# Optimization experiments

Measured on AMD Instinct MI355X. Metric: run time of the kernel, lower is better.

The kernel has to match this reference:

```python
import jax, jax.numpy as jnp
import numpy as np

EPS = 1e-5
PROJ_EPS = 1e-5
MAX_TANH_ARG = 15.0
NUM_LAYERS = 2

def _norm(x):
    return jnp.sqrt(jnp.sum(x * x, axis=-1, keepdims=True))

def log_map_zero(y):
    # Poincare ball log map at the origin: arctanh(||y||) * y / ||y||
    n = _norm(y)
    n_c = jnp.clip(n, EPS, 1.0 - PROJ_EPS)
    return jnp.arctanh(n_c) * y / jnp.maximum(n, EPS)

def exp_map_zero(v):
    # Poincare ball exp map at the origin: tanh(||v||) * v / ||v||
    n = _norm(v)
    n_c = jnp.clip(n, EPS, MAX_TANH_ARG)
    return jnp.tanh(n_c) * v / jnp.maximum(n, EPS)

def setup_inputs() -> dict:
    key = jax.random.key(0)
    k1, k2, k3, k4 = jax.random.split(key, 4)
    N, K, D = 50000, 32, 128
    # scale initial features so they lie inside the unit ball
    node_repr = jax.random.normal(k1, (N, D), dtype=jnp.float32) * 0.01
    adj_mat = jax.random.randint(k2, (N, K), 0, N, dtype=jnp.int32)
    weight = jax.random.uniform(k3, (N, K), dtype=jnp.float32)
    mask = jnp.ones((N, 1), dtype=jnp.float32)
    # learned params: one [D, D] matrix per layer (tie_weight=False, poincare)
    msg_weights = jax.random.normal(k4, (NUM_LAYERS, D, D), dtype=jnp.float32) * (1.0 / np.sqrt(D))
    return {"node_repr": node_repr, "adj_mat": adj_mat, "weight": weight,
            "mask": mask, "msg_weights": msg_weights}

def reference(node_repr, adj_mat, weight, mask, msg_weights):
    x = node_repr
    for step in range(NUM_LAYERS):
        # log map back to tangent space at origin (identity on first layer)
        x = (log_map_zero(x) if step > 0 else x) * mask
        msg = (x @ msg_weights[step]) * mask            # [N, D] dense projection
        nbr = msg[adj_mat]                              # [N, K, D] gather by adjacency
        combined = jnp.einsum('nk,nkd->nd', weight, nbr) * mask  # weighted neighbor sum (dropout p=0)
        x = exp_map_zero(combined) * mask               # back to the manifold
        x = jax.nn.relu(x) * mask                       # poincare activation
    return x
```

## Files before the change

kernel.cpp:

```cpp
#include <hip/hip_runtime.h>

#define EPS 1e-5f
#define PROJ_EPS 1e-5f
#define MAX_TANH_ARG 15.0f

typedef __bf16 bf16x8 __attribute__((ext_vector_type(8)));
typedef float f32x4 __attribute__((ext_vector_type(4)));
typedef float f32x2 __attribute__((ext_vector_type(2)));

__device__ __forceinline__ unsigned short f2bf(float f) {
  unsigned u = __builtin_bit_cast(unsigned, f);
  u += 0x7fffu + ((u >> 16) & 1u);
  return (unsigned short)(u >> 16);
}

union BF8 {
  unsigned short u[8];
  bf16x8 v;
  uint4 q;
};

__global__ __launch_bounds__(256) void prep_kernel(
    const float* __restrict__ W, unsigned short* __restrict__ wpack) {
  const int tid = blockIdx.x * 256 + threadIdx.x;
  if (tid >= 4096) return;
  const int l = tid & 63;
  const int s = (tid >> 6) & 3;
  const int tt = (tid >> 8) & 7;
  const int layer = tid >> 11;
  const int q2 = l >> 4;
  const int n = tt * 16 + (l & 15);
  unsigned short* dst = wpack + ((size_t)((layer * 32 + tt * 4 + s) * 64 + l)) * 8;
  const float* src = W + (size_t)layer * 16384;
#pragma unroll
  for (int j = 0; j < 8; ++j) {
    const int k = s * 32 + q2 * 8 + j;
    dst[j] = f2bf(src[(size_t)k * 128 + n]);
  }
}

__global__ __launch_bounds__(256) void gemm0_kernel(
    const float* __restrict__ xf, const float* __restrict__ mask,
    const unsigned short* __restrict__ wpack, unsigned short* __restrict__ msg,
    const int* __restrict__ adj, const float* __restrict__ wgt,
    unsigned* __restrict__ edges, int nedge, int N, int planeBytes) {
  __shared__ unsigned short tile[64][136];
  const int t = threadIdx.x;
  const int lane = t & 63;
  const int wv = t >> 6;
  const int m = lane & 15;
  const int quad = lane >> 4;
  const int base = blockIdx.x * 64;
  const int wbase = base + wv * 16;

#pragma unroll
  for (int i = 0; i < 8; ++i) {
    const int ge = base * 32 + i * 256 + t;
    if (ge < nedge) {
      const unsigned id = (unsigned)adj[ge] & 0xffffu;
      const unsigned short h = __builtin_bit_cast(unsigned short, (_Float16)wgt[ge]);
      edges[ge] = id | ((unsigned)h << 16);
    }
  }

  {
    const int r = lane >> 2;
    const int c = (lane & 3) * 32;
    const int gr = wbase + r;
    const int grc = gr < N ? gr : N - 1;
    const float4* src = (const float4*)(xf + (size_t)grc * 128 + c);
    unsigned short* drow = &tile[wv * 16 + r][c];
#pragma unroll
    for (int i = 0; i < 8; ++i) {
      const float4 p = src[i];
      drow[i * 4 + 0] = f2bf(p.x);
      drow[i * 4 + 1] = f2bf(p.y);
      drow[i * 4 + 2] = f2bf(p.z);
      drow[i * 4 + 3] = f2bf(p.w);
    }
  }

  f32x4 acc[8];
#pragma unroll
  for (int tt = 0; tt < 8; ++tt) acc[tt] = (f32x4){0.f, 0.f, 0.f, 0.f};
#pragma unroll
  for (int sk = 0; sk < 4; ++sk) {
    BF8 a;
    a.q = *(const uint4*)&tile[wv * 16 + m][sk * 32 + quad * 8];
#pragma unroll
    for (int tt = 0; tt < 8; ++tt) {
      BF8 b;
      b.q = *(const uint4*)(wpack + (size_t)((tt * 4 + sk) * 64 + lane) * 8);
      acc[tt] = __builtin_amdgcn_mfma_f32_16x16x32_bf16(a.v, b.v, acc[tt], 0, 0, 0);
    }
  }

  float sc[4];
#pragma unroll
  for (int r = 0; r < 4; ++r) {
    int rr = wbase + quad * 4 + r;
    rr = rr < N ? rr : N - 1;
    const float s = mask[rr];
    sc[r] = s * s;
  }
#pragma unroll
  for (int tt = 0; tt < 8; ++tt) {
    const int c = tt * 16 + m;
#pragma unroll
    for (int r = 0; r < 4; ++r)
      tile[wv * 16 + quad * 4 + r][c] = f2bf(acc[tt][r] * sc[r]);
  }
  const int r16 = lane >> 2;
  const int sub2 = lane & 3;
  const int grow = wbase + r16;
  if (grow < N) {
#pragma unroll
    for (int p = 0; p < 4; ++p) {
      *(uint4*)((char*)msg + (size_t)p * planeBytes + (size_t)grow * 64 + sub2 * 16) =
          *(const uint4*)((const char*)&tile[wv * 16 + r16][0] + p * 64 + sub2 * 16);
    }
  }
}

__global__ __launch_bounds__(256, 3) void gather_plane_kernel(
    const unsigned short* __restrict__ msg, const unsigned* __restrict__ edges,
    unsigned short* __restrict__ cout, float* __restrict__ scal,
    int N, int planeBytes) {
  __shared__ unsigned ep[64 * 36];
  const int t = threadIdx.x;
  const int p = blockIdx.x & 3;
  const int nbase = (blockIdx.x >> 2) * 64;

  for (int e = t; e < 64 * 32; e += 256) {
    const int node = e >> 5, k = e & 31;
    const int gn = nbase + node;
    ep[node * 36 + k] = (gn < N) ? edges[(size_t)gn * 32 + k] : 0u;
  }
  __syncthreads();

  const int node = t >> 2;
  const int sub = t & 3;
  const int gnode = nbase + node;
  const unsigned* mp = ep + node * 36;
  const char* plane = (const char*)msg + (size_t)p * planeBytes;
  const int suboff = sub * 16;

  unsigned ew[32];
#pragma unroll
  for (int i = 0; i < 8; ++i)
    *(uint4*)&ew[4 * i] = *(const uint4*)(mp + 4 * i);

  f32x2 acc[4];
#pragma unroll
  for (int d = 0; d < 4; ++d) acc[d] = (f32x2){0.f, 0.f};

  uint4 q[16];
#pragma unroll
  for (int k = 0; k < 16; ++k)
    q[k] = *(const uint4*)(plane + ((size_t)(ew[k] & 0xffffu) * 64 + suboff));

#pragma unroll
  for (int k = 0; k < 16; ++k) {
    const float w = (float)__builtin_bit_cast(_Float16, (unsigned short)(ew[k] >> 16));
    const f32x2 w2 = {w, w};
    const uint4 qq = q[k];
    q[k] = *(const uint4*)(plane + ((size_t)(ew[16 + k] & 0xffffu) * 64 + suboff));
#pragma unroll
    for (int d = 0; d < 4; ++d) {
      const unsigned qd = (&qq.x)[d];
      f32x2 v2;
      v2.x = __builtin_bit_cast(float, qd << 16);
      v2.y = __builtin_bit_cast(float, qd & 0xffff0000u);
      acc[d] = __builtin_elementwise_fma(v2, w2, acc[d]);
    }
  }
#pragma unroll
  for (int k = 0; k < 16; ++k) {
    const float w = (float)__builtin_bit_cast(_Float16,
                                              (unsigned short)(ew[16 + k] >> 16));
    const f32x2 w2 = {w, w};
#pragma unroll
    for (int d = 0; d < 4; ++d) {
      const unsigned qd = (&q[k].x)[d];
      f32x2 v2;
      v2.x = __builtin_bit_cast(float, qd << 16);
      v2.y = __builtin_bit_cast(float, qd & 0xffff0000u);
      acc[d] = __builtin_elementwise_fma(v2, w2, acc[d]);
    }
  }

  float s_all = 0.f, s_rel = 0.f;
  uint4 pk4;
  unsigned* pw = &pk4.x;
#pragma unroll
  for (int d = 0; d < 4; ++d) {
    s_all = fmaf(acc[d].x, acc[d].x, s_all);
    s_all = fmaf(acc[d].y, acc[d].y, s_all);
    const float r0 = fmaxf(acc[d].x, 0.f);
    const float r1 = fmaxf(acc[d].y, 0.f);
    s_rel = fmaf(r0, r0, s_rel);
    s_rel = fmaf(r1, r1, s_rel);
    pw[d] = (unsigned)f2bf(r0) | ((unsigned)f2bf(r1) << 16);
  }
  s_all += __shfl_xor(s_all, 1);
  s_all += __shfl_xor(s_all, 2);
  s_rel += __shfl_xor(s_rel, 1);
  s_rel += __shfl_xor(s_rel, 2);

  if (gnode < N) {
    *(uint4*)((char*)cout + (size_t)p * planeBytes + (size_t)gnode * 64 + suboff) = pk4;
    if (sub == 0)
      *(float2*)(scal + (size_t)gnode * 8 + p * 2) = make_float2(s_all, s_rel);
  }
}

__global__ __launch_bounds__(256) void gemm1_kernel(
    const unsigned short* __restrict__ cA, const float* __restrict__ scalA,
    const float* __restrict__ mask, const unsigned short* __restrict__ wpack2,
    unsigned short* __restrict__ msg, int N, int planeBytes) {
  __shared__ unsigned short tile[64][136];
  const int lane = threadIdx.x & 63;
  const int wv = threadIdx.x >> 6;
  const int m = lane & 15;
  const int quad = lane >> 4;
  const int wbase = blockIdx.x * 64 + wv * 16;
  const int row = wbase + m;
  const int rowc = row < N ? row : N - 1;

  f32x4 acc[8];
#pragma unroll
  for (int tt = 0; tt < 8; ++tt) acc[tt] = (f32x4){0.f, 0.f, 0.f, 0.f};
#pragma unroll
  for (int sk = 0; sk < 4; ++sk) {
    BF8 a;
    a.q = *(const uint4*)((const char*)cA + (size_t)sk * planeBytes +
                          (size_t)rowc * 64 + quad * 16);
#pragma unroll
    for (int tt = 0; tt < 8; ++tt) {
      BF8 b;
      b.q = *(const uint4*)(wpack2 + (size_t)((tt * 4 + sk) * 64 + lane) * 8);
      acc[tt] = __builtin_amdgcn_mfma_f32_16x16x32_bf16(a.v, b.v, acc[tt], 0, 0, 0);
    }
  }

  float sc[4];
#pragma unroll
  for (int r = 0; r < 4; ++r) {
    int rr = wbase + quad * 4 + r;
    rr = rr < N ? rr : N - 1;
    const float* s8 = scalA + (size_t)rr * 8;
    const float S_all = s8[0] + s8[2] + s8[4] + s8[6];
    const float S_rel = s8[1] + s8[3] + s8[5] + s8[7];
    const float mm = mask[rr];
    const float s2 = mm * mm * S_all;
    const float nrm = sqrtf(s2);
    const float ncl = fminf(fmaxf(nrm, EPS), MAX_TANH_ARG);
    const float f1 = tanhf(ncl) / fmaxf(nrm, EPS) * mm * mm * mm;
    const float r2 = f1 * f1 * S_rel;
    const float nr = sqrtf(r2);
    const float nc2 = fminf(fmaxf(nr, EPS), 1.0f - PROJ_EPS);
    const float ls = 0.5f * logf((1.f + nc2) / (1.f - nc2)) / fmaxf(nr, EPS);
    sc[r] = ls * mm * mm * f1;
  }
#pragma unroll
  for (int tt = 0; tt < 8; ++tt) {
    const int c = tt * 16 + m;
#pragma unroll
    for (int r = 0; r < 4; ++r)
      tile[wv * 16 + quad * 4 + r][c] = f2bf(acc[tt][r] * sc[r]);
  }
  const int r16 = lane >> 2;
  const int sub2 = lane & 3;
  const int grow = wbase + r16;
  if (grow < N) {
#pragma unroll
    for (int p = 0; p < 4; ++p) {
      *(uint4*)((char*)msg + (size_t)p * planeBytes + (size_t)grow * 64 + sub2 * 16) =
          *(const uint4*)((const char*)&tile[wv * 16 + r16][0] + p * 64 + sub2 * 16);
    }
  }
}

__global__ __launch_bounds__(256) void final_kernel(
    const unsigned short* __restrict__ cB, const float* __restrict__ scalB,
    const float* __restrict__ mask, float* __restrict__ out,
    int N, int planeBytes) {
  const int t = threadIdx.x;
  const int node = t >> 2;
  const int sub = t & 3;
  const int gnode = blockIdx.x * 64 + node;
  if (gnode >= N) return;
  const float* s8 = scalB + (size_t)gnode * 8;
  const float S_all = s8[0] + s8[2] + s8[4] + s8[6];
  const float mm = mask[gnode];
  const float s2 = mm * mm * S_all;
  const float nrm = sqrtf(s2);
  const float ncl = fminf(fmaxf(nrm, EPS), MAX_TANH_ARG);
  const float f2 = tanhf(ncl) / fmaxf(nrm, EPS) * mm * mm * mm;
#pragma unroll
  for (int p = 0; p < 4; ++p) {
    const uint4 q = *(const uint4*)((const char*)cB + (size_t)p * planeBytes +
                                    (size_t)gnode * 64 + sub * 16);
    float4 o0, o1;
    o0.x = f2 * __builtin_bit_cast(float, q.x << 16);
    o0.y = f2 * __builtin_bit_cast(float, q.x & 0xffff0000u);
    o0.z = f2 * __builtin_bit_cast(float, q.y << 16);
    o0.w = f2 * __builtin_bit_cast(float, q.y & 0xffff0000u);
    o1.x = f2 * __builtin_bit_cast(float, q.z << 16);
    o1.y = f2 * __builtin_bit_cast(float, q.z & 0xffff0000u);
    o1.z = f2 * __builtin_bit_cast(float, q.w << 16);
    o1.w = f2 * __builtin_bit_cast(float, q.w & 0xffff0000u);
    const int cb = p * 32 + sub * 8;
    *(float4*)(out + (size_t)gnode * 128 + cb) = o0;
    *(float4*)(out + (size_t)gnode * 128 + cb + 4) = o1;
  }
}

extern "C" void kernel_launch(void* const* d_in, const int* in_sizes, int n_in,
                              void* d_out, int out_size, void* d_ws, size_t ws_size,
                              hipStream_t stream) {
  const float* node = (const float*)d_in[0];
  const int* adj = (const int*)d_in[1];
  const float* wgt = (const float*)d_in[2];
  const float* mask = (const float*)d_in[3];
  const float* mw = (const float*)d_in[4];
  float* out = (float*)d_out;
  const int N = in_sizes[0] / 128;
  const int gb = (N + 63) / 64;
  const int planeBytes = gb * 64 * 64;
  const int nedge = N * 32;

  unsigned short* msg = (unsigned short*)d_out;
  unsigned* edges = (unsigned*)((char*)d_out + (size_t)4 * planeBytes);
  float* scalA = (float*)((char*)d_out + (size_t)4 * planeBytes + (size_t)nedge * 4);
  unsigned short* wpack = (unsigned short*)d_ws;
  unsigned short* cAB = (unsigned short*)((char*)d_ws + 65536);
  float* scalB = (float*)((char*)d_ws + 65536 + (size_t)4 * planeBytes);

  hipLaunchKernelGGL(prep_kernel, dim3(16), dim3(256), 0, stream, mw, wpack);
  hipLaunchKernelGGL(gemm0_kernel, dim3(gb), dim3(256), 0, stream,
                     node, mask, wpack, msg, adj, wgt, edges, nedge, N, planeBytes);
  hipLaunchKernelGGL(gather_plane_kernel, dim3(gb * 4), dim3(256), 0, stream,
                     msg, edges, cAB, scalA, N, planeBytes);
  hipLaunchKernelGGL(gemm1_kernel, dim3(gb), dim3(256), 0, stream,
                     cAB, scalA, mask, wpack + 16384, msg, N, planeBytes);
  hipLaunchKernelGGL(gather_plane_kernel, dim3(gb * 4), dim3(256), 0, stream,
                     msg, edges, cAB, scalB, N, planeBytes);
  hipLaunchKernelGGL(final_kernel, dim3(gb), dim3(256), 0, stream,
                     cAB, scalB, mask, out, N, planeBytes);
}
```

Measured before the change: 199.0 us.

## Fuse neighbor aggregation with layer-1 GEMM and with final exp-map epilogue

```diff
diff --git a/kernel.cpp b/kernel.cpp
--- a/kernel.cpp
+++ b/kernel.cpp
@@ -122,49 +122,64 @@
   }
 }
 
-__global__ __launch_bounds__(256, 3) void gather_plane_kernel(
+__global__ __launch_bounds__(256, 3) void agg_gemm1_kernel(
     const unsigned short* __restrict__ msg, const unsigned* __restrict__ edges,
-    unsigned short* __restrict__ cout, float* __restrict__ scal,
-    int N, int planeBytes) {
+    const float* __restrict__ mask, const unsigned short* __restrict__ wpack2,
+    unsigned short* __restrict__ msg2, int N, int planeBytes) {
   __shared__ unsigned ep[64 * 36];
+  __shared__ unsigned short tile[64][136];
+  __shared__ float sAll[64];
+  __shared__ float sRel[64];
   const int t = threadIdx.x;
-  const int p = blockIdx.x & 3;
-  const int nbase = (blockIdx.x >> 2) * 64;
-
-  for (int e = t; e < 64 * 32; e += 256) {
-    const int node = e >> 5, k = e & 31;
-    const int gn = nbase + node;
-    ep[node * 36 + k] = (gn < N) ? edges[(size_t)gn * 32 + k] : 0u;
-  }
-  __syncthreads();
-
-  const int node = t >> 2;
-  const int sub = t & 3;
-  const int gnode = nbase + node;
-  const unsigned* mp = ep + node * 36;
-  const char* plane = (const char*)msg + (size_t)p * planeBytes;
+  const int lane = t & 63;
+  const int wv = t >> 6;
+  const int nbase = blockIdx.x * 64;
+  const int wrow0 = wv * 16;
+  const int pstart = blockIdx.x & 3;
+
+#pragma unroll
+  for (int i = 0; i < 2; ++i) {
+    const int idx = lane + i * 64;
+    const int row = idx >> 3;
+    const int qd = idx & 7;
+    const int gn = nbase + wrow0 + row;
+    uint4 v = {0u, 0u, 0u, 0u};
+    if (gn < N) v = *(const uint4*)(edges + (size_t)gn * 32 + qd * 4);
+    *(uint4*)&ep[(wrow0 + row) * 36 + qd * 4] = v;
+  }
+
+  const int node = lane >> 2;
+  const int sub = lane & 3;
   const int suboff = sub * 16;
-
+  const unsigned* mp = ep + (wrow0 + node) * 36;
   unsigned ew[32];
 #pragma unroll
-  for (int i = 0; i < 8; ++i)
-    *(uint4*)&ew[4 * i] = *(const uint4*)(mp + 4 * i);
+  for (int i = 0; i < 8; ++i) *(uint4*)&ew[4 * i] = *(const uint4*)(mp + 4 * i);
+
+  const char* pb[4];
+#pragma unroll
+  for (int ph = 0; ph < 4; ++ph)
+    pb[ph] = (const char*)msg + (size_t)((pstart + ph) & 3) * planeBytes;
 
   f32x2 acc[4];
 #pragma unroll
   for (int d = 0; d < 4; ++d) acc[d] = (f32x2){0.f, 0.f};
+  float s_all = 0.f, s_rel = 0.f;
 
   uint4 q[16];
 #pragma unroll
-  for (int k = 0; k < 16; ++k)
-    q[k] = *(const uint4*)(plane + ((size_t)(ew[k] & 0xffffu) * 64 + suboff));
-
-#pragma unroll
-  for (int k = 0; k < 16; ++k) {
+  for (int e = 0; e < 16; ++e)
+    q[e] = *(const uint4*)(pb[e >> 5] + ((ew[e & 31] & 0xffffu) * 64 + suboff));
+
+#pragma unroll
+  for (int e = 0; e < 128; ++e) {
+    const int k = e & 31;
     const float w = (float)__builtin_bit_cast(_Float16, (unsigned short)(ew[k] >> 16));
     const f32x2 w2 = {w, w};
-    const uint4 qq = q[k];
-    q[k] = *(const uint4*)(plane + ((size_t)(ew[16 + k] & 0xffffu) * 64 + suboff));
+    const uint4 qq = q[e & 15];
+    const int en = e + 16;
+    if (en < 128)
+      q[e & 15] = *(const uint4*)(pb[en >> 5] + ((ew[en & 31] & 0xffffu) * 64 + suboff));
 #pragma unroll
     for (int d = 0; d < 4; ++d) {
       const unsigned qd = (&qq.x)[d];
@@ -173,85 +188,60 @@
       v2.y = __builtin_bit_cast(float, qd & 0xffff0000u);
       acc[d] = __builtin_elementwise_fma(v2, w2, acc[d]);
     }
-  }
-#pragma unroll
-  for (int k = 0; k < 16; ++k) {
-    const float w = (float)__builtin_bit_cast(_Float16,
-                                              (unsigned short)(ew[16 + k] >> 16));
-    const f32x2 w2 = {w, w};
-#pragma unroll
-    for (int d = 0; d < 4; ++d) {
-      const unsigned qd = (&q[k].x)[d];
-      f32x2 v2;
-      v2.x = __builtin_bit_cast(float, qd << 16);
-      v2.y = __builtin_bit_cast(float, qd & 0xffff0000u);
-      acc[d] = __builtin_elementwise_fma(v2, w2, acc[d]);
-    }
-  }
-
-  float s_all = 0.f, s_rel = 0.f;
-  uint4 pk4;
-  unsigned* pw = &pk4.x;
-#pragma unroll
-  for (int d = 0; d < 4; ++d) {
-    s_all = fmaf(acc[d].x, acc[d].x, s_all);
-    s_all = fmaf(acc[d].y, acc[d].y, s_all);
-    const float r0 = fmaxf(acc[d].x, 0.f);
-    const float r1 = fmaxf(acc[d].y, 0.f);
-    s_rel = fmaf(r0, r0, s_rel);
-    s_rel = fmaf(r1, r1, s_rel);
-    pw[d] = (unsigned)f2bf(r0) | ((unsigned)f2bf(r1) << 16);
-  }
+    if (k == 31) {
+      const int p = (pstart + (e >> 5)) & 3;
+      uint4 pk4;
+      unsigned* pw = &pk4.x;
+#pragma unroll
+      for (int d = 0; d < 4; ++d) {
+        s_all = fmaf(acc[d].x, acc[d].x, s_all);
+        s_all = fmaf(acc[d].y, acc[d].y, s_all);
+        const float r0 = fmaxf(acc[d].x, 0.f);
+        const float r1 = fmaxf(acc[d].y, 0.f);
+        s_rel = fmaf(r0, r0, s_rel);
+        s_rel = fmaf(r1, r1, s_rel);
+        pw[d] = (unsigned)f2bf(r0) | ((unsigned)f2bf(r1) << 16);
+        acc[d] = (f32x2){0.f, 0.f};
+      }
+      *(uint4*)&tile[wrow0 + node][p * 32 + sub * 8] = pk4;
+    }
+  }
+
   s_all += __shfl_xor(s_all, 1);
   s_all += __shfl_xor(s_all, 2);
   s_rel += __shfl_xor(s_rel, 1);
   s_rel += __shfl_xor(s_rel, 2);
-
-  if (gnode < N) {
-    *(uint4*)((char*)cout + (size_t)p * planeBytes + (size_t)gnode * 64 + suboff) = pk4;
-    if (sub == 0)
-      *(float2*)(scal + (size_t)gnode * 8 + p * 2) = make_float2(s_all, s_rel);
-  }
-}
-
-__global__ __launch_bounds__(256) void gemm1_kernel(
-    const unsigned short* __restrict__ cA, const float* __restrict__ scalA,
-    const float* __restrict__ mask, const unsigned short* __restrict__ wpack2,
-    unsigned short* __restrict__ msg, int N, int planeBytes) {
-  __shared__ unsigned short tile[64][136];
-  const int lane = threadIdx.x & 63;
-  const int wv = threadIdx.x >> 6;
+  if (sub == 0) {
+    sAll[wrow0 + node] = s_all;
+    sRel[wrow0 + node] = s_rel;
+  }
+
   const int m = lane & 15;
   const int quad = lane >> 4;
-  const int wbase = blockIdx.x * 64 + wv * 16;
-  const int row = wbase + m;
-  const int rowc = row < N ? row : N - 1;
-
-  f32x4 acc[8];
-#pragma unroll
-  for (int tt = 0; tt < 8; ++tt) acc[tt] = (f32x4){0.f, 0.f, 0.f, 0.f};
+  f32x4 gacc[8];
+#pragma unroll
+  for (int tt = 0; tt < 8; ++tt) gacc[tt] = (f32x4){0.f, 0.f, 0.f, 0.f};
 #pragma unroll
   for (int sk = 0; sk < 4; ++sk) {
     BF8 a;
-    a.q = *(const uint4*)((const char*)cA + (size_t)sk * planeBytes +
-                          (size_t)rowc * 64 + quad * 16);
+    a.q = *(const uint4*)&tile[wrow0 + m][sk * 32 + quad * 8];
 #pragma unroll
     for (int tt = 0; tt < 8; ++tt) {
       BF8 b;
       b.q = *(const uint4*)(wpack2 + (size_t)((tt * 4 + sk) * 64 + lane) * 8);
-      acc[tt] = __builtin_amdgcn_mfma_f32_16x16x32_bf16(a.v, b.v, acc[tt], 0, 0, 0);
+      gacc[tt] = __builtin_amdgcn_mfma_f32_16x16x32_bf16(a.v, b.v, gacc[tt], 0, 0, 0);
     }
   }
 
   float sc[4];
 #pragma unroll
   for (int r = 0; r < 4; ++r) {
-    int rr = wbase + quad * 4 + r;
+    const int lr = wrow0 + quad * 4 + r;
+    int rr = nbase + lr;
     rr = rr < N ? rr : N - 1;
-    const float* s8 = scalA + (size_t)rr * 8;
-    const float S_all = s8[0] + s8[2] + s8[4] + s8[6];
-    const float S_rel = s8[1] + s8[3] + s8[5] + s8[7];
     const float mm = mask[rr];
+    const float S_all = sAll[lr];
+    const float S_rel = sRel[lr];
     const float s2 = mm * mm * S_all;
     const float nrm = sqrtf(s2);
     const float ncl = fminf(fmaxf(nrm, EPS), MAX_TANH_ARG);
@@ -267,52 +257,119 @@
     const int c = tt * 16 + m;
 #pragma unroll
     for (int r = 0; r < 4; ++r)
-      tile[wv * 16 + quad * 4 + r][c] = f2bf(acc[tt][r] * sc[r]);
+      tile[wrow0 + quad * 4 + r][c] = f2bf(gacc[tt][r] * sc[r]);
   }
   const int r16 = lane >> 2;
   const int sub2 = lane & 3;
-  const int grow = wbase + r16;
+  const int grow = nbase + wrow0 + r16;
   if (grow < N) {
 #pragma unroll
     for (int p = 0; p < 4; ++p) {
-      *(uint4*)((char*)msg + (size_t)p * planeBytes + (size_t)grow * 64 + sub2 * 16) =
-          *(const uint4*)((const char*)&tile[wv * 16 + r16][0] + p * 64 + sub2 * 16);
-    }
-  }
-}
-
-__global__ __launch_bounds__(256) void final_kernel(
-    const unsigned short* __restrict__ cB, const float* __restrict__ scalB,
-    const float* __restrict__ mask, float* __restrict__ out,
-    int N, int planeBytes) {
+      *(uint4*)((char*)msg2 + (size_t)p * planeBytes + (size_t)grow * 64 + sub2 * 16) =
+          *(const uint4*)((const char*)&tile[wrow0 + r16][0] + p * 64 + sub2 * 16);
+    }
+  }
+}
+
+__global__ __launch_bounds__(256, 3) void agg_final_kernel(
+    const unsigned short* __restrict__ msg2, const unsigned* __restrict__ edges,
+    const float* __restrict__ mask, float* __restrict__ out, int N,
+    int planeBytes) {
+  __shared__ unsigned ep[64 * 36];
   const int t = threadIdx.x;
-  const int node = t >> 2;
-  const int sub = t & 3;
-  const int gnode = blockIdx.x * 64 + node;
-  if (gnode >= N) return;
-  const float* s8 = scalB + (size_t)gnode * 8;
-  const float S_all = s8[0] + s8[2] + s8[4] + s8[6];
-  const float mm = mask[gnode];
-  const float s2 = mm * mm * S_all;
+  const int lane = t & 63;
+  const int wv = t >> 6;
+  const int nbase = blockIdx.x * 64;
+  const int wrow0 = wv * 16;
+  const int pstart = blockIdx.x & 3;
+
+#pragma unroll
+  for (int i = 0; i < 2; ++i) {
+    const int idx = lane + i * 64;
+    const int row = idx >> 3;
+    const int qd = idx & 7;
+    const int gn = nbase + wrow0 + row;
+    uint4 v = {0u, 0u, 0u, 0u};
+    if (gn < N) v = *(const uint4*)(edges + (size_t)gn * 32 + qd * 4);
+    *(uint4*)&ep[(wrow0 + row) * 36 + qd * 4] = v;
+  }
+
+  const int node = lane >> 2;
+  const int sub = lane & 3;
+  const int suboff = sub * 16;
+  const unsigned* mp = ep + (wrow0 + node) * 36;
+  unsigned ew[32];
+#pragma unroll
+  for (int i = 0; i < 8; ++i) *(uint4*)&ew[4 * i] = *(const uint4*)(mp + 4 * i);
+
+  const char* pb[4];
+#pragma unroll
+  for (int ph = 0; ph < 4; ++ph)
+    pb[ph] = (const char*)msg2 + (size_t)((pstart + ph) & 3) * planeBytes;
+
+  f32x2 acc[16];
+#pragma unroll
+  for (int i = 0; i < 16; ++i) acc[i] = (f32x2){0.f, 0.f};
+
+  uint4 q[16];
+#pragma unroll
+  for (int e = 0; e < 16; ++e)
+    q[e] = *(const uint4*)(pb[e >> 5] + ((ew[e & 31] & 0xffffu) * 64 + suboff));
+
+#pragma unroll
+  for (int e = 0; e < 128; ++e) {
+    const int k = e & 31;
+    const int ph = e >> 5;
+    const float w = (float)__builtin_bit_cast(_Float16, (unsigned short)(ew[k] >> 16));
+    const f32x2 w2 = {w, w};
+    const uint4 qq = q[e & 15];
+    const int en = e + 16;
+    if (en < 128)
+      q[e & 15] = *(const uint4*)(pb[en >> 5] + ((ew[en & 31] & 0xffffu) * 64 + suboff));
+#pragma unroll
+    for (int d = 0; d < 4; ++d) {
+      const unsigned qd = (&qq.x)[d];
+      f32x2 v2;
+      v2.x = __builtin_bit_cast(float, qd << 16);
+      v2.y = __builtin_bit_cast(float, qd & 0xffff0000u);
+      acc[ph * 4 + d] = __builtin_elementwise_fma(v2, w2, acc[ph * 4 + d]);
+    }
+  }
+
+  float s_all = 0.f;
+#pragma unroll
+  for (int i = 0; i < 16; ++i) {
+    s_all = fmaf(acc[i].x, acc[i].x, s_all);
+    s_all = fmaf(acc[i].y, acc[i].y, s_all);
+  }
+  s_all += __shfl_xor(s_all, 1);
+  s_all += __shfl_xor(s_all, 2);
+
+  const int gnode = nbase + wrow0 + node;
+  const int gnc = gnode < N ? gnode : N - 1;
+  const float mm = mask[gnc];
+  const float s2 = mm * mm * s_all;
   const float nrm = sqrtf(s2);
   const float ncl = fminf(fmaxf(nrm, EPS), MAX_TANH_ARG);
   const float f2 = tanhf(ncl) / fmaxf(nrm, EPS) * mm * mm * mm;
-#pragma unroll
-  for (int p = 0; p < 4; ++p) {
-    const uint4 q = *(const uint4*)((const char*)cB + (size_t)p * planeBytes +
-                                    (size_t)gnode * 64 + sub * 16);
-    float4 o0, o1;
-    o0.x = f2 * __builtin_bit_cast(float, q.x << 16);
-    o0.y = f2 * __builtin_bit_cast(float, q.x & 0xffff0000u);
-    o0.z = f2 * __builtin_bit_cast(float, q.y << 16);
-    o0.w = f2 * __builtin_bit_cast(float, q.y & 0xffff0000u);
-    o1.x = f2 * __builtin_bit_cast(float, q.z << 16);
-    o1.y = f2 * __builtin_bit_cast(float, q.z & 0xffff0000u);
-    o1.z = f2 * __builtin_bit_cast(float, q.w << 16);
-    o1.w = f2 * __builtin_bit_cast(float, q.w & 0xffff0000u);
-    const int cb = p * 32 + sub * 8;
-    *(float4*)(out + (size_t)gnode * 128 + cb) = o0;
-    *(float4*)(out + (size_t)gnode * 128 + cb + 4) = o1;
+
+  if (gnode < N) {
+    float* orow = out + (size_t)gnode * 128;
+#pragma unroll
+    for (int ph = 0; ph < 4; ++ph) {
+      const int p = (pstart + ph) & 3;
+      float4 o0, o1;
+      o0.x = f2 * fmaxf(acc[ph * 4 + 0].x, 0.f);
+      o0.y = f2 * fmaxf(acc[ph * 4 + 0].y, 0.f);
+      o0.z = f2 * fmaxf(acc[ph * 4 + 1].x, 0.f);
+      o0.w = f2 * fmaxf(acc[ph * 4 + 1].y, 0.f);
+      o1.x = f2 * fmaxf(acc[ph * 4 + 2].x, 0.f);
+      o1.y = f2 * fmaxf(acc[ph * 4 + 2].y, 0.f);
+      o1.z = f2 * fmaxf(acc[ph * 4 + 3].x, 0.f);
+      o1.w = f2 * fmaxf(acc[ph * 4 + 3].y, 0.f);
+      *(float4*)(orow + p * 32 + sub * 8) = o0;
+      *(float4*)(orow + p * 32 + sub * 8 + 4) = o1;
+    }
   }
 }
 
@@ -330,22 +387,16 @@
   const int planeBytes = gb * 64 * 64;
   const int nedge = N * 32;
 
-  unsigned short* msg = (unsigned short*)d_out;
-  unsigned* edges = (unsigned*)((char*)d_out + (size_t)4 * planeBytes);
-  float* scalA = (float*)((char*)d_out + (size_t)4 * planeBytes + (size_t)nedge * 4);
+  unsigned short* msg1 = (unsigned short*)d_out;
   unsigned short* wpack = (unsigned short*)d_ws;
-  unsigned short* cAB = (unsigned short*)((char*)d_ws + 65536);
-  float* scalB = (float*)((char*)d_ws + 65536 + (size_t)4 * planeBytes);
+  unsigned short* msg2 = (unsigned short*)((char*)d_ws + 65536);
+  unsigned* edges = (unsigned*)((char*)d_ws + 65536 + (size_t)4 * planeBytes);
 
   hipLaunchKernelGGL(prep_kernel, dim3(16), dim3(256), 0, stream, mw, wpack);
   hipLaunchKernelGGL(gemm0_kernel, dim3(gb), dim3(256), 0, stream,
-                     node, mask, wpack, msg, adj, wgt, edges, nedge, N, planeBytes);
-  hipLaunchKernelGGL(gather_plane_kernel, dim3(gb * 4), dim3(256), 0, stream,
-                     msg, edges, cAB, scalA, N, planeBytes);
-  hipLaunchKernelGGL(gemm1_kernel, dim3(gb), dim3(256), 0, stream,
-                     cAB, scalA, mask, wpack + 16384, msg, N, planeBytes);
-  hipLaunchKernelGGL(gather_plane_kernel, dim3(gb * 4), dim3(256), 0, stream,
-                     msg, edges, cAB, scalB, N, planeBytes);
-  hipLaunchKernelGGL(final_kernel, dim3(gb), dim3(256), 0, stream,
-                     cAB, scalB, mask, out, N, planeBytes);
-}
+                     node, mask, wpack, msg1, adj, wgt, edges, nedge, N, planeBytes);
+  hipLaunchKernelGGL(agg_gemm1_kernel, dim3(gb), dim3(256), 0, stream,
+                     msg1, edges, mask, wpack + 16384, msg2, N, planeBytes);
+  hipLaunchKernelGGL(agg_final_kernel, dim3(gb), dim3(256), 0, stream,
+                     msg2, edges, mask, out, N, planeBytes);
+}
```

After: 396.1 us. +99.0%, slower.

## Reorder gather before GEMM using linearity and fuse norms into GEMM epilogues

Applied to the files above, without the earlier changes.

```diff
diff --git a/kernel.cpp b/kernel.cpp
--- a/kernel.cpp
+++ b/kernel.cpp
@@ -7,6 +7,7 @@
 typedef __bf16 bf16x8 __attribute__((ext_vector_type(8)));
 typedef float f32x4 __attribute__((ext_vector_type(4)));
 typedef float f32x2 __attribute__((ext_vector_type(2)));
+typedef unsigned u32x4 __attribute__((ext_vector_type(4)));
 
 __device__ __forceinline__ unsigned short f2bf(float f) {
   unsigned u = __builtin_bit_cast(unsigned, f);
@@ -39,19 +40,13 @@
   }
 }
 
-__global__ __launch_bounds__(256) void gemm0_kernel(
+__global__ __launch_bounds__(256) void stage_kernel(
     const float* __restrict__ xf, const float* __restrict__ mask,
-    const unsigned short* __restrict__ wpack, unsigned short* __restrict__ msg,
-    const int* __restrict__ adj, const float* __restrict__ wgt,
-    unsigned* __restrict__ edges, int nedge, int N, int planeBytes) {
-  __shared__ unsigned short tile[64][136];
+    unsigned short* __restrict__ planes, const int* __restrict__ adj,
+    const float* __restrict__ wgt, unsigned* __restrict__ edges,
+    int nedge, int N, int planeBytes) {
   const int t = threadIdx.x;
-  const int lane = t & 63;
-  const int wv = t >> 6;
-  const int m = lane & 15;
-  const int quad = lane >> 4;
   const int base = blockIdx.x * 64;
-  const int wbase = base + wv * 16;
 
 #pragma unroll
   for (int i = 0; i < 8; ++i) {
@@ -63,69 +58,30 @@
     }
   }
 
-  {
-    const int r = lane >> 2;
-    const int c = (lane & 3) * 32;
-    const int gr = wbase + r;
-    const int grc = gr < N ? gr : N - 1;
-    const float4* src = (const float4*)(xf + (size_t)grc * 128 + c);
-    unsigned short* drow = &tile[wv * 16 + r][c];
-#pragma unroll
-    for (int i = 0; i < 8; ++i) {
-      const float4 p = src[i];
-      drow[i * 4 + 0] = f2bf(p.x);
-      drow[i * 4 + 1] = f2bf(p.y);
-      drow[i * 4 + 2] = f2bf(p.z);
-      drow[i * 4 + 3] = f2bf(p.w);
-    }
-  }
-
-  f32x4 acc[8];
-#pragma unroll
-  for (int tt = 0; tt < 8; ++tt) acc[tt] = (f32x4){0.f, 0.f, 0.f, 0.f};
-#pragma unroll
-  for (int sk = 0; sk < 4; ++sk) {
-    BF8 a;
-    a.q = *(const uint4*)&tile[wv * 16 + m][sk * 32 + quad * 8];
-#pragma unroll
-    for (int tt = 0; tt < 8; ++tt) {
-      BF8 b;
-      b.q = *(const uint4*)(wpack + (size_t)((tt * 4 + sk) * 64 + lane) * 8);
-      acc[tt] = __builtin_amdgcn_mfma_f32_16x16x32_bf16(a.v, b.v, acc[tt], 0, 0, 0);
-    }
-  }
-
-  float sc[4];
-#pragma unroll
-  for (int r = 0; r < 4; ++r) {
-    int rr = wbase + quad * 4 + r;
-    rr = rr < N ? rr : N - 1;
-    const float s = mask[rr];
-    sc[r] = s * s;
-  }
-#pragma unroll
-  for (int tt = 0; tt < 8; ++tt) {
-    const int c = tt * 16 + m;
-#pragma unroll
-    for (int r = 0; r < 4; ++r)
-      tile[wv * 16 + quad * 4 + r][c] = f2bf(acc[tt][r] * sc[r]);
-  }
-  const int r16 = lane >> 2;
-  const int sub2 = lane & 3;
-  const int grow = wbase + r16;
-  if (grow < N) {
-#pragma unroll
-    for (int p = 0; p < 4; ++p) {
-      *(uint4*)((char*)msg + (size_t)p * planeBytes + (size_t)grow * 64 + sub2 * 16) =
-          *(const uint4*)((const char*)&tile[wv * 16 + r16][0] + p * 64 + sub2 * 16);
-    }
-  }
-}
-
-__global__ __launch_bounds__(256, 3) void gather_plane_kernel(
+  const int node = t >> 2;
+  const int sub = t & 3;
+  const int gnode = base + node;
+  if (gnode >= N) return;
+  const float mm = mask[gnode];
+  const float s2 = mm * mm;
+  const float* src = xf + (size_t)gnode * 128 + sub * 32;
+  char* drow = (char*)planes + (size_t)sub * planeBytes + (size_t)gnode * 64;
+#pragma unroll
+  for (int i = 0; i < 4; ++i) {
+    const f32x4 a = *(const f32x4*)(src + i * 8);
+    const f32x4 b = *(const f32x4*)(src + i * 8 + 4);
+    u32x4 pk;
+    pk[0] = (unsigned)f2bf(a.x * s2) | ((unsigned)f2bf(a.y * s2) << 16);
+    pk[1] = (unsigned)f2bf(a.z * s2) | ((unsigned)f2bf(a.w * s2) << 16);
+    pk[2] = (unsigned)f2bf(b.x * s2) | ((unsigned)f2bf(b.y * s2) << 16);
+    pk[3] = (unsigned)f2bf(b.z * s2) | ((unsigned)f2bf(b.w * s2) << 16);
+    *(u32x4*)(drow + i * 16) = pk;
+  }
+}
+
+__global__ __launch_bounds__(256, 3) void gather_kernel(
     const unsigned short* __restrict__ msg, const unsigned* __restrict__ edges,
-    unsigned short* __restrict__ cout, float* __restrict__ scal,
-    int N, int planeBytes) {
+    unsigned short* __restrict__ gout, int N, int planeBytes) {
   __shared__ unsigned ep[64 * 36];
   const int t = threadIdx.x;
   const int p = blockIdx.x & 3;
@@ -189,35 +145,19 @@
     }
   }
 
-  float s_all = 0.f, s_rel = 0.f;
-  uint4 pk4;
-  unsigned* pw = &pk4.x;
-#pragma unroll
-  for (int d = 0; d < 4; ++d) {
-    s_all = fmaf(acc[d].x, acc[d].x, s_all);
-    s_all = fmaf(acc[d].y, acc[d].y, s_all);
-    const float r0 = fmaxf(acc[d].x, 0.f);
-    const float r1 = fmaxf(acc[d].y, 0.f);
-    s_rel = fmaf(r0, r0, s_rel);
-    s_rel = fmaf(r1, r1, s_rel);
-    pw[d] = (unsigned)f2bf(r0) | ((unsigned)f2bf(r1) << 16);
-  }
-  s_all += __shfl_xor(s_all, 1);
-  s_all += __shfl_xor(s_all, 2);
-  s_rel += __shfl_xor(s_rel, 1);
-  s_rel += __shfl_xor(s_rel, 2);
-
   if (gnode < N) {
-    *(uint4*)((char*)cout + (size_t)p * planeBytes + (size_t)gnode * 64 + suboff) = pk4;
-    if (sub == 0)
-      *(float2*)(scal + (size_t)gnode * 8 + p * 2) = make_float2(s_all, s_rel);
-  }
-}
-
-__global__ __launch_bounds__(256) void gemm1_kernel(
-    const unsigned short* __restrict__ cA, const float* __restrict__ scalA,
-    const float* __restrict__ mask, const unsigned short* __restrict__ wpack2,
-    unsigned short* __restrict__ msg, int N, int planeBytes) {
+    u32x4 pk4;
+#pragma unroll
+    for (int d = 0; d < 4; ++d)
+      pk4[d] = (unsigned)f2bf(acc[d].x) | ((unsigned)f2bf(acc[d].y) << 16);
+    *(u32x4*)((char*)gout + (size_t)p * planeBytes + (size_t)gnode * 64 + suboff) = pk4;
+  }
+}
+
+__global__ __launch_bounds__(256) void gemmA_kernel(
+    const unsigned short* __restrict__ g, const float* __restrict__ mask,
+    const unsigned short* __restrict__ wpackL, unsigned short* __restrict__ planesOut,
+    int N, int planeBytes) {
   __shared__ unsigned short tile[64][136];
   const int lane = threadIdx.x & 63;
   const int wv = threadIdx.x >> 6;
@@ -233,13 +173,36 @@
 #pragma unroll
   for (int sk = 0; sk < 4; ++sk) {
     BF8 a;
-    a.q = *(const uint4*)((const char*)cA + (size_t)sk * planeBytes +
+    a.q = *(const uint4*)((const char*)g + (size_t)sk * planeBytes +
                           (size_t)rowc * 64 + quad * 16);
 #pragma unroll
     for (int tt = 0; tt < 8; ++tt) {
       BF8 b;
-      b.q = *(const uint4*)(wpack2 + (size_t)((tt * 4 + sk) * 64 + lane) * 8);
+      b.q = *(const uint4*)(wpackL + (size_t)((tt * 4 + sk) * 64 + lane) * 8);
       acc[tt] = __builtin_amdgcn_mfma_f32_16x16x32_bf16(a.v, b.v, acc[tt], 0, 0, 0);
+    }
+  }
+
+  float sa[4], sr[4];
+#pragma unroll
+  for (int r = 0; r < 4; ++r) {
+    float a = 0.f, rl = 0.f;
+#pragma unroll
+    for (int tt = 0; tt < 8; ++tt) {
+      const float v = acc[tt][r];
+      a = fmaf(v, v, a);
+      const float rv = fmaxf(v, 0.f);
+      rl = fmaf(rv, rv, rl);
+    }
+    sa[r] = a;
+    sr[r] = rl;
+  }
+#pragma unroll
+  for (int msk = 1; msk < 16; msk <<= 1) {
+#pragma unroll
+    for (int r = 0; r < 4; ++r) {
+      sa[r] += __shfl_xor(sa[r], msk);
+      sr[r] += __shfl_xor(sr[r], msk);
     }
   }
 
@@ -248,15 +211,12 @@
   for (int r = 0; r < 4; ++r) {
     int rr = wbase + quad * 4 + r;
     rr = rr < N ? rr : N - 1;
-    const float* s8 = scalA + (size_t)rr * 8;
-    const float S_all = s8[0] + s8[2] + s8[4] + s8[6];
-    const float S_rel = s8[1] + s8[3] + s8[5] + s8[7];
     const float mm = mask[rr];
-    const float s2 = mm * mm * S_all;
+    const float s2 = mm * mm * sa[r];
     const float nrm = sqrtf(s2);
     const float ncl = fminf(fmaxf(nrm, EPS), MAX_TANH_ARG);
     const float f1 = tanhf(ncl) / fmaxf(nrm, EPS) * mm * mm * mm;
-    const float r2 = f1 * f1 * S_rel;
+    const float r2 = f1 * f1 * sr[r];
     const float nr = sqrtf(r2);
     const float nc2 = fminf(fmaxf(nr, EPS), 1.0f - PROJ_EPS);
     const float ls = 0.5f * logf((1.f + nc2) / (1.f - nc2)) / fmaxf(nr, EPS);
@@ -267,7 +227,7 @@
     const int c = tt * 16 + m;
 #pragma unroll
     for (int r = 0; r < 4; ++r)
-      tile[wv * 16 + quad * 4 + r][c] = f2bf(acc[tt][r] * sc[r]);
+      tile[wv * 16 + quad * 4 + r][c] = f2bf(fmaxf(acc[tt][r], 0.f) * sc[r]);
   }
   const int r16 = lane >> 2;
   const int sub2 = lane & 3;
@@ -275,44 +235,82 @@
   if (grow < N) {
 #pragma unroll
     for (int p = 0; p < 4; ++p) {
-      *(uint4*)((char*)msg + (size_t)p * planeBytes + (size_t)grow * 64 + sub2 * 16) =
+      *(uint4*)((char*)planesOut + (size_t)p * planeBytes + (size_t)grow * 64 + sub2 * 16) =
           *(const uint4*)((const char*)&tile[wv * 16 + r16][0] + p * 64 + sub2 * 16);
     }
   }
 }
 
-__global__ __launch_bounds__(256) void final_kernel(
-    const unsigned short* __restrict__ cB, const float* __restrict__ scalB,
-    const float* __restrict__ mask, float* __restrict__ out,
+__global__ __launch_bounds__(256) void gemmB_kernel(
+    const unsigned short* __restrict__ g, const float* __restrict__ mask,
+    const unsigned short* __restrict__ wpackL, float* __restrict__ out,
     int N, int planeBytes) {
-  const int t = threadIdx.x;
-  const int node = t >> 2;
-  const int sub = t & 3;
-  const int gnode = blockIdx.x * 64 + node;
-  if (gnode >= N) return;
-  const float* s8 = scalB + (size_t)gnode * 8;
-  const float S_all = s8[0] + s8[2] + s8[4] + s8[6];
-  const float mm = mask[gnode];
-  const float s2 = mm * mm * S_all;
-  const float nrm = sqrtf(s2);
-  const float ncl = fminf(fmaxf(nrm, EPS), MAX_TANH_ARG);
-  const float f2 = tanhf(ncl) / fmaxf(nrm, EPS) * mm * mm * mm;
-#pragma unroll
-  for (int p = 0; p < 4; ++p) {
-    const uint4 q = *(const uint4*)((const char*)cB + (size_t)p * planeBytes +
-                                    (size_t)gnode * 64 + sub * 16);
-    float4 o0, o1;
-    o0.x = f2 * __builtin_bit_cast(float, q.x << 16);
-    o0.y = f2 * __builtin_bit_cast(float, q.x & 0xffff0000u);
-    o0.z = f2 * __builtin_bit_cast(float, q.y << 16);
-    o0.w = f2 * __builtin_bit_cast(float, q.y & 0xffff0000u);
-    o1.x = f2 * __builtin_bit_cast(float, q.z << 16);
-    o1.y = f2 * __builtin_bit_cast(float, q.z & 0xffff0000u);
-    o1.z = f2 * __builtin_bit_cast(float, q.w << 16);
-    o1.w = f2 * __builtin_bit_cast(float, q.w & 0xffff0000u);
-    const int cb = p * 32 + sub * 8;
-    *(float4*)(out + (size_t)gnode * 128 + cb) = o0;
-    *(float4*)(out + (size_t)gnode * 128 + cb + 4) = o1;
+  __shared__ float otile[64][132];
+  const int lane = threadIdx.x & 63;
+  const int wv = threadIdx.x >> 6;
+  const int m = lane & 15;
+  const int quad = lane >> 4;
+  const int wbase = blockIdx.x * 64 + wv * 16;
+  const int row = wbase + m;
+  const int rowc = row < N ? row : N - 1;
+
+  f32x4 acc[8];
+#pragma unroll
+  for (int tt = 0; tt < 8; ++tt) acc[tt] = (f32x4){0.f, 0.f, 0.f, 0.f};
+#pragma unroll
+  for (int sk = 0; sk < 4; ++sk) {
+    BF8 a;
+    a.q = *(const uint4*)((const char*)g + (size_t)sk * planeBytes +
+                          (size_t)rowc * 64 + quad * 16);
+#pragma unroll
+    for (int tt = 0; tt < 8; ++tt) {
+      BF8 b;
+      b.q = *(const uint4*)(wpackL + (size_t)((tt * 4 + sk) * 64 + lane) * 8);
+      acc[tt] = __builtin_amdgcn_mfma_f32_16x16x32_bf16(a.v, b.v, acc[tt], 0, 0, 0);
+    }
+  }
+
+  float sa[4];
+#pragma unroll
+  for (int r = 0; r < 4; ++r) {
+    float a = 0.f;
+#pragma unroll
+    for (int tt = 0; tt < 8; ++tt) a = fmaf(acc[tt][r], acc[tt][r], a);
+    sa[r] = a;
+  }
+#pragma unroll
+  for (int msk = 1; msk < 16; msk <<= 1) {
+#pragma unroll
+    for (int r = 0; r < 4; ++r) sa[r] += __shfl_xor(sa[r], msk);
+  }
+
+  float f2s[4];
+#pragma unroll
+  for (int r = 0; r < 4; ++r) {
+    int rr = wbase + quad * 4 + r;
+    rr = rr < N ? rr : N - 1;
+    const float mm = mask[rr];
+    const float s2 = mm * mm * sa[r];
+    const float nrm = sqrtf(s2);
+    const float ncl = fminf(fmaxf(nrm, EPS), MAX_TANH_ARG);
+    f2s[r] = tanhf(ncl) / fmaxf(nrm, EPS) * mm * mm * mm;
+  }
+#pragma unroll
+  for (int tt = 0; tt < 8; ++tt) {
+    const int c = tt * 16 + m;
+#pragma unroll
+    for (int r = 0; r < 4; ++r)
+      otile[wv * 16 + quad * 4 + r][c] = f2s[r] * fmaxf(acc[tt][r], 0.f);
+  }
+  const int r16 = lane >> 2;
+  const int sub2 = lane & 3;
+  const int grow = wbase + r16;
+  if (grow < N) {
+    float* orow = out + (size_t)grow * 128 + sub2 * 32;
+    const float* srow = &otile[wv * 16 + r16][sub2 * 32];
+#pragma unroll
+    for (int i = 0; i < 8; ++i)
+      *(f32x4*)(orow + i * 4) = *(const f32x4*)(srow + i * 4);
   }
 }
 
@@ -330,22 +328,20 @@
   const int planeBytes = gb * 64 * 64;
   const int nedge = N * 32;
 
-  unsigned short* msg = (unsigned short*)d_out;
-  unsigned* edges = (unsigned*)((char*)d_out + (size_t)4 * planeBytes);
-  float* scalA = (float*)((char*)d_out + (size_t)4 * planeBytes + (size_t)nedge * 4);
+  unsigned short* xyplanes = (unsigned short*)d_out;
   unsigned short* wpack = (unsigned short*)d_ws;
-  unsigned short* cAB = (unsigned short*)((char*)d_ws + 65536);
-  float* scalB = (float*)((char*)d_ws + 65536 + (size_t)4 * planeBytes);
+  unsigned short* gplanes = (unsigned short*)((char*)d_ws + 65536);
+  unsigned* edges = (unsigned*)((char*)d_ws + 65536 + (size_t)4 * planeBytes);
 
   hipLaunchKernelGGL(prep_kernel, dim3(16), dim3(256), 0, stream, mw, wpack);
-  hipLaunchKernelGGL(gemm0_kernel, dim3(gb), dim3(256), 0, stream,
-                     node, mask, wpack, msg, adj, wgt, edges, nedge, N, planeBytes);
-  hipLaunchKernelGGL(gather_plane_kernel, dim3(gb * 4), dim3(256), 0, stream,
-                     msg, edges, cAB, scalA, N, planeBytes);
-  hipLaunchKernelGGL(gemm1_kernel, dim3(gb), dim3(256), 0, stream,
-                     cAB, scalA, mask, wpack + 16384, msg, N, planeBytes);
-  hipLaunchKernelGGL(gather_plane_kernel, dim3(gb * 4), dim3(256), 0, stream,
-                     msg, edges, cAB, scalB, N, planeBytes);
-  hipLaunchKernelGGL(final_kernel, dim3(gb), dim3(256), 0, stream,
-                     cAB, scalB, mask, out, N, planeBytes);
-}
+  hipLaunchKernelGGL(stage_kernel, dim3(gb), dim3(256), 0, stream,
+                     node, mask, xyplanes, adj, wgt, edges, nedge, N, planeBytes);
+  hipLaunchKernelGGL(gather_kernel, dim3(gb * 4), dim3(256), 0, stream,
+                     xyplanes, edges, gplanes, N, planeBytes);
+  hipLaunchKernelGGL(gemmA_kernel, dim3(gb), dim3(256), 0, stream,
+                     gplanes, mask, wpack, xyplanes, N, planeBytes);
+  hipLaunchKernelGGL(gather_kernel, dim3(gb * 4), dim3(256), 0, stream,
+                     xyplanes, edges, gplanes, N, planeBytes);
+  hipLaunchKernelGGL(gemmB_kernel, dim3(gb), dim3(256), 0, stream,
+                     gplanes, mask, wpack + 16384, out, N, planeBytes);
+}
```

Measured after the change: 628.7 us. +215.9%, slower.
